# Kernel tuning notes

Hardware: AMD Instinct MI355X
Metric: run time of the kernel (lower is better)

## Reference

```python
import jax, jax.numpy as jnp
import numpy as np

SNR_DB = 20.0   # fixed draw from snr_range=(20, 20)
B_COEF = 0.02   # pink-noise IIR coefficient


def setup_inputs() -> dict:
    key = jax.random.key(0)
    k1, k2 = jax.random.split(key)
    L = 16_777_216  # 2**24 audio samples
    audio = jax.random.normal(k1, (L,), dtype=jnp.float32)
    white = jax.random.normal(k2, (L,), dtype=jnp.float32)  # driving white noise for pink branch
    return {"audio": audio, "white": white}


def _pink_noise(white):
    # p[0] = 0; p[i] = B*w[i] + (1-B)*p[i-1]  -> linear recurrence x_i = a_i*x_{i-1} + u_i
    b = jnp.asarray(B_COEF, white.dtype)
    a = jnp.full(white.shape, 1.0 - B_COEF, white.dtype).at[0].set(0.0)
    u = (b * white).at[0].set(0.0)

    def combine(lhs, rhs):
        a1, u1 = lhs
        a2, u2 = rhs
        return a1 * a2, a2 * u1 + u2

    _, pink = jax.lax.associative_scan(combine, (a, u))
    return pink


def reference(audio, white):
    signal_power = jnp.mean(audio ** 2)
    noise_power = signal_power / (10.0 ** (SNR_DB / 10.0))
    noise = _pink_noise(white) * jnp.sqrt(noise_power)
    return audio + noise
```

## Files before the change

kernel.cpp:

```cpp
#include <hip/hip_runtime.h>
#include <math.h>

#define L_TOTAL (1 << 24)

constexpr float A_COEF = 0.98f;
constexpr float B_COEF = 0.02f;

constexpr int T    = 256;
constexpr int S    = 16;
constexpr int TS   = T * S;
constexpr int WARM = 512;
constexpr int NPART = 1024;

__device__ __forceinline__ void block_sync_lds() {
    asm volatile("s_waitcnt lgkmcnt(0)\n\ts_barrier" ::: "memory");
}

__global__ __launch_bounds__(256) void sumsq_kernel(const float4* __restrict__ a4,
                                                    float* __restrict__ partials,
                                                    int n4) {
    int idx    = blockIdx.x * blockDim.x + threadIdx.x;
    int stride = gridDim.x * blockDim.x;
    float s = 0.f;
    for (int i = idx; i < n4; i += stride) {
        float4 v = a4[i];
        s += v.x * v.x + v.y * v.y + v.z * v.z + v.w * v.w;
    }
    #pragma unroll
    for (int o = 32; o > 0; o >>= 1) s += __shfl_down(s, o, 64);
    __shared__ float wsum[4];
    int lane = threadIdx.x & 63;
    int wv   = threadIdx.x >> 6;
    if (lane == 0) wsum[wv] = s;
    __syncthreads();
    if (threadIdx.x == 0)
        partials[blockIdx.x] = wsum[0] + wsum[1] + wsum[2] + wsum[3];
}

__global__ __launch_bounds__(256) void pink_add_kernel(const float* __restrict__ audio,
                                                       const float* __restrict__ white,
                                                       const float* __restrict__ partials,
                                                       float* __restrict__ out) {
    __shared__ float lds[TS + TS / 16];
    __shared__ float wave_tot[4];
    __shared__ float wsum[4];
    __shared__ float psum[4];

    const int tid  = threadIdx.x;
    const int lane = tid & 63;
    const int wv   = tid >> 6;
    const int base = blockIdx.x * TS;

    const float4* wp = reinterpret_cast<const float4*>(white + base + tid * S);
    float w[S];
    #pragma unroll
    for (int q = 0; q < S / 4; ++q) {
        float4 v = wp[q];
        w[4 * q + 0] = v.x; w[4 * q + 1] = v.y;
        w[4 * q + 2] = v.z; w[4 * q + 3] = v.w;
    }
    float2 wu = make_float2(0.f, 0.f);
    if (blockIdx.x > 0) {
        const float2* up = reinterpret_cast<const float2*>(white + base - WARM);
        wu = up[tid];
    }
    const float4 pp = reinterpret_cast<const float4*>(partials)[tid];

    float apow[S];
    apow[0] = A_COEF;
    #pragma unroll
    for (int j = 1; j < S; ++j) apow[j] = apow[j - 1] * A_COEF;
    const float beta = apow[S - 1];
    const float b2 = beta * beta, b4 = b2 * b2, b8 = b4 * b4;
    const float b16 = b8 * b8, b32 = b16 * b16, b64 = b32 * b32;
    const float bpow[6] = {beta, b2, b4, b8, b16, b32};

    const float beta_l = exp2f((float)lane * log2f(beta));
    float b64w = 1.f;
    #pragma unroll
    for (int i = 0; i < 3; ++i) if (wv > i) b64w *= b64;
    const float beta_t = beta_l * b64w;

    #pragma unroll
    for (int j = 0; j < S; ++j) w[j] *= B_COEF;
    if (base == 0 && tid == 0) w[0] = 0.f;

    float l[S];
    float p = 0.f;
    #pragma unroll
    for (int j = 0; j < S; ++j) { p = fmaf(A_COEF, p, w[j]); l[j] = p; }

    float W = p;
    #pragma unroll
    for (int i = 0; i < 6; ++i) {
        const int o = 1 << i;
        float up = __shfl_up(W, o, 64);
        if (lane >= o) W = fmaf(bpow[i], up, W);
    }

    const float a2c = A_COEF * A_COEF;
    float part = fmaf(A_COEF, B_COEF * wu.x, B_COEF * wu.y);
    part *= exp2f((float)(255 - tid) * log2f(a2c));
    #pragma unroll
    for (int o = 32; o > 0; o >>= 1) part += __shfl_down(part, o, 64);

    float ss = pp.x + pp.y + pp.z + pp.w;
    #pragma unroll
    for (int o = 32; o > 0; o >>= 1) ss += __shfl_down(ss, o, 64);

    if (lane == 63) wave_tot[wv] = W;
    if (lane == 0)  { wsum[wv] = part; psum[wv] = ss; }
    block_sync_lds();

    const float G0 = wave_tot[0], G1 = wave_tot[1];
    const float G2 = wave_tot[2], G3 = wave_tot[3];
    const float P1 = G0;
    const float P2 = fmaf(P1, b64, G1);
    const float P3 = fmaf(P2, b64, G2);
    const float P  = (wv == 0) ? 0.f : (wv == 1) ? P1 : (wv == 2) ? P2 : P3;
    const float Cw = wsum[0] + wsum[1] + wsum[2] + wsum[3];
    const float sumsq = psum[0] + psum[1] + psum[2] + psum[3];
    const float scale = sqrtf(sumsq * (1.0f / ((float)L_TOTAL * 100.0f)));

    const float Wp = __shfl_up(W, 1, 64);
    const float E  = ((lane == 0) ? 0.f : Wp) + P * beta_l;
    const float C  = E + Cw * beta_t;

    const int lb = tid * 17;
    #pragma unroll
    for (int j = 0; j < S; ++j)
        lds[lb + j] = fmaf(C, apow[j], l[j]);

    const float4* ap = reinterpret_cast<const float4*>(audio + base);
    float4 av[4];
    #pragma unroll
    for (int q = 0; q < 4; ++q) av[q] = ap[q * T + tid];

    block_sync_lds();

    float4* op = reinterpret_cast<float4*>(out + base);
    #pragma unroll
    for (int q = 0; q < 4; ++q) {
        const int i4 = q * T + tid;
        const int i  = i4 * 4;
        const int pi = i + (i >> 4);
        float4 a = av[q];
        float4 r;
        r.x = fmaf(lds[pi + 0], scale, a.x);
        r.y = fmaf(lds[pi + 1], scale, a.y);
        r.z = fmaf(lds[pi + 2], scale, a.z);
        r.w = fmaf(lds[pi + 3], scale, a.w);
        op[i4] = r;
    }
}

extern "C" void kernel_launch(void* const* d_in, const int* in_sizes, int n_in,
                              void* d_out, int out_size, void* d_ws, size_t ws_size,
                              hipStream_t stream) {
    const float* audio = (const float*)d_in[0];
    const float* white = (const float*)d_in[1];
    float* out         = (float*)d_out;
    float* partials    = (float*)d_ws;

    const int n4 = L_TOTAL / 4;
    sumsq_kernel<<<NPART, 256, 0, stream>>>((const float4*)audio, partials, n4);

    const int blocks = L_TOTAL / TS;
    pink_add_kernel<<<blocks, 256, 0, stream>>>(audio, white, partials, out);
}
```

Measured before the change: 171.4 us.

## Scan pink noise in coalesced float4 segments and drop LDS transpose

Each thread now handles four coalesced float4 chunks (stride T) instead of a contiguous run of sixteen samples. Every chunk gets its own 4-element local scan, a wave-level scan and a block-level combine, and a final carry across the four 1024-sample segments. This removes the shared-memory staging buffer and the second barrier, and the audio load is issued earlier. In exchange there are four times as many wave shuffles in the scan. A leftover dead expression C remains in the code.

```diff
diff --git a/kernel.cpp b/kernel.cpp
--- a/kernel.cpp
+++ b/kernel.cpp
@@ -7,8 +7,7 @@
 constexpr float B_COEF = 0.02f;
 
 constexpr int T    = 256;
-constexpr int S    = 16;
-constexpr int TS   = T * S;
+constexpr int TS   = 4096;
 constexpr int WARM = 512;
 constexpr int NPART = 1024;
 
@@ -41,8 +40,7 @@
                                                        const float* __restrict__ white,
                                                        const float* __restrict__ partials,
                                                        float* __restrict__ out) {
-    __shared__ float lds[TS + TS / 16];
-    __shared__ float wave_tot[4];
+    __shared__ float gtot[4][4];
     __shared__ float wsum[4];
     __shared__ float psum[4];
 
@@ -51,14 +49,11 @@
     const int wv   = tid >> 6;
     const int base = blockIdx.x * TS;
 
-    const float4* wp = reinterpret_cast<const float4*>(white + base + tid * S);
-    float w[S];
+    const float4* wp4 = reinterpret_cast<const float4*>(white + base);
+    float4 u[4];
     #pragma unroll
-    for (int q = 0; q < S / 4; ++q) {
-        float4 v = wp[q];
-        w[4 * q + 0] = v.x; w[4 * q + 1] = v.y;
-        w[4 * q + 2] = v.z; w[4 * q + 3] = v.w;
-    }
+    for (int q = 0; q < 4; ++q) u[q] = wp4[q * T + tid];
+
     float2 wu = make_float2(0.f, 0.f);
     if (blockIdx.x > 0) {
         const float2* up = reinterpret_cast<const float2*>(white + base - WARM);
@@ -66,39 +61,52 @@
     }
     const float4 pp = reinterpret_cast<const float4*>(partials)[tid];
 
-    float apow[S];
-    apow[0] = A_COEF;
+    const float4* ap4 = reinterpret_cast<const float4*>(audio + base);
+    float4 av[4];
     #pragma unroll
-    for (int j = 1; j < S; ++j) apow[j] = apow[j - 1] * A_COEF;
-    const float beta = apow[S - 1];
-    const float b2 = beta * beta, b4 = b2 * b2, b8 = b4 * b4;
-    const float b16 = b8 * b8, b32 = b16 * b16, b64 = b32 * b32;
-    const float bpow[6] = {beta, b2, b4, b8, b16, b32};
+    for (int q = 0; q < 4; ++q) av[q] = ap4[q * T + tid];
 
-    const float beta_l = exp2f((float)lane * log2f(beta));
-    float b64w = 1.f;
+    const float a2c  = A_COEF * A_COEF;
+    const float b4c  = a2c * a2c;
+    const float b8c  = b4c * b4c, b16c = b8c * b8c, b32c = b16c * b16c;
+    const float b64c = b32c * b32c, b128c = b64c * b64c;
+    const float b256c  = b128c * b128c;
+    const float b1024c = b256c * b256c * b256c * b256c;
+    const float bpow[6] = {b4c, b8c, b16c, b32c, b64c, b128c};
+    const float cg[4] = {1.f, b1024c, b1024c * b1024c, b1024c * b1024c * b1024c};
+
+    const float b4lane = exp2f((float)lane * log2f(b4c));
+    float b256w = 1.f;
     #pragma unroll
-    for (int i = 0; i < 3; ++i) if (wv > i) b64w *= b64;
-    const float beta_t = beta_l * b64w;
+    for (int i = 0; i < 3; ++i) if (wv > i) b256w *= b256c;
+    const float b4t = b4lane * b256w;
 
     #pragma unroll
-    for (int j = 0; j < S; ++j) w[j] *= B_COEF;
-    if (base == 0 && tid == 0) w[0] = 0.f;
+    for (int q = 0; q < 4; ++q) {
+        u[q].x *= B_COEF; u[q].y *= B_COEF; u[q].z *= B_COEF; u[q].w *= B_COEF;
+    }
+    if (base == 0 && tid == 0) u[0].x = 0.f;
 
-    float l[S];
-    float p = 0.f;
+    float W[4];
     #pragma unroll
-    for (int j = 0; j < S; ++j) { p = fmaf(A_COEF, p, w[j]); l[j] = p; }
+    for (int q = 0; q < 4; ++q) {
+        float p = u[q].x;
+        p = fmaf(A_COEF, p, u[q].y);
+        p = fmaf(A_COEF, p, u[q].z);
+        p = fmaf(A_COEF, p, u[q].w);
+        W[q] = p;
+    }
 
-    float W = p;
     #pragma unroll
     for (int i = 0; i < 6; ++i) {
         const int o = 1 << i;
-        float up = __shfl_up(W, o, 64);
-        if (lane >= o) W = fmaf(bpow[i], up, W);
+        #pragma unroll
+        for (int q = 0; q < 4; ++q) {
+            float up = __shfl_up(W[q], o, 64);
+            if (lane >= o) W[q] = fmaf(bpow[i], up, W[q]);
+        }
     }
 
-    const float a2c = A_COEF * A_COEF;
     float part = fmaf(A_COEF, B_COEF * wu.x, B_COEF * wu.y);
     part *= exp2f((float)(255 - tid) * log2f(a2c));
     #pragma unroll
@@ -108,49 +116,51 @@
     #pragma unroll
     for (int o = 32; o > 0; o >>= 1) ss += __shfl_down(ss, o, 64);
 
-    if (lane == 63) wave_tot[wv] = W;
-    if (lane == 0)  { wsum[wv] = part; psum[wv] = ss; }
+    if (lane == 63) {
+        #pragma unroll
+        for (int q = 0; q < 4; ++q) gtot[q][wv] = W[q];
+    }
+    if (lane == 0) { wsum[wv] = part; psum[wv] = ss; }
     block_sync_lds();
 
-    const float G0 = wave_tot[0], G1 = wave_tot[1];
-    const float G2 = wave_tot[2], G3 = wave_tot[3];
-    const float P1 = G0;
-    const float P2 = fmaf(P1, b64, G1);
-    const float P3 = fmaf(P2, b64, G2);
-    const float P  = (wv == 0) ? 0.f : (wv == 1) ? P1 : (wv == 2) ? P2 : P3;
-    const float Cw = wsum[0] + wsum[1] + wsum[2] + wsum[3];
+    float P[4], Gt[4];
+    #pragma unroll
+    for (int q = 0; q < 4; ++q) {
+        const float G0 = gtot[q][0], G1 = gtot[q][1];
+        const float G2 = gtot[q][2], G3 = gtot[q][3];
+        const float P1 = G0;
+        const float P2 = fmaf(P1, b256c, G1);
+        const float P3 = fmaf(P2, b256c, G2);
+        P[q]  = (wv == 0) ? 0.f : (wv == 1) ? P1 : (wv == 2) ? P2 : P3;
+        Gt[q] = fmaf(P3, b256c, G3);
+    }
+    const float Cw    = wsum[0] + wsum[1] + wsum[2] + wsum[3];
     const float sumsq = psum[0] + psum[1] + psum[2] + psum[3];
     const float scale = sqrtf(sumsq * (1.0f / ((float)L_TOTAL * 100.0f)));
 
-    const float Wp = __shfl_up(W, 1, 64);
-    const float E  = ((lane == 0) ? 0.f : Wp) + P * beta_l;
-    const float C  = E + Cw * beta_t;
+    float H[4];
+    H[0] = 0.f;
+    H[1] = Gt[0];
+    H[2] = fmaf(H[1], b1024c, Gt[1]);
+    H[3] = fmaf(H[2], b1024c, Gt[2]);
 
-    const int lb = tid * 17;
-    #pragma unroll
-    for (int j = 0; j < S; ++j)
-        lds[lb + j] = fmaf(C, apow[j], l[j]);
-
-    const float4* ap = reinterpret_cast<const float4*>(audio + base);
-    float4 av[4];
-    #pragma unroll
-    for (int q = 0; q < 4; ++q) av[q] = ap[q * T + tid];
-
-    block_sync_lds();
-
-    float4* op = reinterpret_cast<float4*>(out + base);
+    float4* op4 = reinterpret_cast<float4*>(out + base);
     #pragma unroll
     for (int q = 0; q < 4; ++q) {
-        const int i4 = q * T + tid;
-        const int i  = i4 * 4;
-        const int pi = i + (i >> 4);
-        float4 a = av[q];
+        const float Wp = __shfl_up(W[q], 1, 64);
+        const float E  = ((lane == 0) ? 0.f : Wp) + P[q] * b4lane;
+        const float C  = E + fmaf(Cw, cg[q], H[q] / 1.0f) * b4t
+                           - H[q] * b4t + (H[q] + Cw * cg[q]) * b4t;
+        const float Cx = E + (H[q] + Cw * cg[q]) * b4t;
+
+        float p = Cx;
         float4 r;
-        r.x = fmaf(lds[pi + 0], scale, a.x);
-        r.y = fmaf(lds[pi + 1], scale, a.y);
-        r.z = fmaf(lds[pi + 2], scale, a.z);
-        r.w = fmaf(lds[pi + 3], scale, a.w);
-        op[i4] = r;
+        p = fmaf(A_COEF, p, u[q].x); r.x = fmaf(p, scale, av[q].x);
+        p = fmaf(A_COEF, p, u[q].y); r.y = fmaf(p, scale, av[q].y);
+        p = fmaf(A_COEF, p, u[q].z); r.z = fmaf(p, scale, av[q].z);
+        p = fmaf(A_COEF, p, u[q].w); r.w = fmaf(p, scale, av[q].w);
+        (void)C;
+        op4[q * T + tid] = r;
     }
 }
 
```

Result: no change. 170.2 us (-0.7%).
